# Performance work log

Measured on AMD Instinct MI355X. Metric: run time of the kernel, lower is better.

Reference implementation:

```python
import jax, jax.numpy as jnp
import numpy as np

NEG_SLOPE = 0.2  # PyG GATConv default leaky_relu slope


def gat_conv(x, ei, W, a_src, a_dst, b, heads, ch):
    """One PyG-style GATConv (eval mode, add_self_loops already applied to ei)."""
    N = x.shape[0]
    h = (x @ W).reshape(N, heads, ch)                      # [N,H,C]
    src, dst = ei[0], ei[1]
    al_s = jnp.sum(h * a_src, axis=-1)                     # [N,H]
    al_d = jnp.sum(h * a_dst, axis=-1)                     # [N,H]
    e = jax.nn.leaky_relu(al_s[src] + al_d[dst], NEG_SLOPE)  # [E,H]
    m = jax.ops.segment_max(e, dst, num_segments=N)        # stable softmax over in-edges
    ex = jnp.exp(e - m[dst])
    den = jax.ops.segment_sum(ex, dst, num_segments=N)
    alpha = ex / den[dst]                                  # [E,H]
    msg = alpha[:, :, None] * h[src]                       # [E,H,C]
    out = jax.ops.segment_sum(msg, dst, num_segments=N)    # [N,H,C]
    return out.reshape(N, heads * ch) + b


def setup_inputs() -> dict:
    key = jax.random.key(0)
    ks = jax.random.split(key, 12)
    N, E, D_in, C, H, D_out = 10000, 320000, 256, 128, 4, 64
    HC = H * C

    def glorot(k, shape):
        fan = shape[0] + shape[-1]
        return jax.random.normal(k, shape, dtype=jnp.float32) * np.sqrt(2.0 / fan)

    x = jax.random.normal(ks[0], (N, D_in), dtype=jnp.float32)
    edge_index = jax.random.randint(ks[1], (2, E), 0, N, dtype=jnp.int64)
    return {
        "x": x,
        "edge_index": edge_index,
        "W1": glorot(ks[2], (D_in, HC)),
        "a_src1": glorot(ks[3], (H, C)),
        "a_dst1": glorot(ks[4], (H, C)),
        "b1": jnp.zeros((HC,), dtype=jnp.float32),
        "W2": glorot(ks[5], (HC, HC)),
        "a_src2": glorot(ks[6], (H, C)),
        "a_dst2": glorot(ks[7], (H, C)),
        "b2": jnp.zeros((HC,), dtype=jnp.float32),
        "W3": glorot(ks[8], (HC, D_out)),
        "a_src3": glorot(ks[9], (1, D_out)),
        "a_dst3": glorot(ks[10], (1, D_out)),
        "b3": jnp.zeros((D_out,), dtype=jnp.float32),
    }


def reference(x, edge_index, W1, a_src1, a_dst1, b1, W2, a_src2, a_dst2, b2,
              W3, a_src3, a_dst3, b3):
    N = x.shape[0]
    loops = jnp.arange(N, dtype=edge_index.dtype)
    ei = jnp.concatenate([edge_index, jnp.stack([loops, loops])], axis=1)
    H, C = a_src1.shape
    h = jax.nn.elu(gat_conv(x, ei, W1, a_src1, a_dst1, b1, H, C))
    h = jax.nn.elu(gat_conv(h, ei, W2, a_src2, a_dst2, b2, H, C))
    out = gat_conv(h, ei, W3, a_src3, a_dst3, b3, 1, a_src3.shape[1])
    return out
```

## Files before the change

### kernel.cpp

```cpp
#include <hip/hip_runtime.h>
#include <hip/hip_fp16.h>

typedef _Float16 f16x8 __attribute__((ext_vector_type(8)));
typedef float f32x4 __attribute__((ext_vector_type(4)));

__device__ __forceinline__ unsigned short f2h_bits(float f) {
    __half h = __float2half(f);
    return *reinterpret_cast<unsigned short*>(&h);
}
__device__ __forceinline__ float h2f_bits(unsigned short u) {
    __half h = *reinterpret_cast<__half*>(&u);
    return __half2float(h);
}

__device__ __forceinline__ void fma_mix_lo(float& acc, float a, unsigned hw) {
    asm("v_fma_mix_f32 %0, %1, %2, %0 op_sel_hi:[0,1,0]"
        : "+v"(acc) : "v"(a), "v"(hw));
}
__device__ __forceinline__ void fma_mix_hi(float& acc, float a, unsigned hw) {
    asm("v_fma_mix_f32 %0, %1, %2, %0 op_sel:[0,1,0] op_sel_hi:[0,1,0]"
        : "+v"(acc) : "v"(a), "v"(hw));
}

__device__ __forceinline__ void gload_lds16(const void* g, void* l) {
    __builtin_amdgcn_global_load_lds(
        (const __attribute__((address_space(1))) unsigned int*)g,
        (__attribute__((address_space(3))) unsigned int*)l, 16, 0, 0);
}

__global__ void k_prep(const float* __restrict__ W1, unsigned short* __restrict__ W1T,
                       const float* __restrict__ W2, unsigned short* __restrict__ W2T,
                       const float* __restrict__ W3, unsigned short* __restrict__ W3T,
                       const float* __restrict__ x, unsigned short* __restrict__ xb,
                       int* __restrict__ csr, int Mcap,
                       const int* __restrict__ ei, int E, int* __restrict__ deg,
                       int DIN, int HC, int DOUT, int N)
{
    int i = blockIdx.x * blockDim.x + threadIdx.x;
    int n1 = DIN * HC;
    int n2 = n1 + HC * HC;
    int n3 = n2 + HC * DOUT;
    int n4 = n3 + N * DIN;
    int n5 = n4 + Mcap;
    int n6 = n5 + E;
    if (i < n1) {
        int k = i / HC, n = i - k * HC;
        W1T[n * DIN + k] = f2h_bits(W1[i]);
    } else if (i < n2) {
        int j = i - n1;
        int k = j / HC, n = j - k * HC;
        W2T[n * HC + k] = f2h_bits(W2[j]);
    } else if (i < n3) {
        int j = i - n2;
        int k = j / DOUT, n = j - k * DOUT;
        W3T[n * HC + k] = f2h_bits(W3[j]);
    } else if (i < n4) {
        int j = i - n3;
        xb[j] = f2h_bits(x[j]);
    } else if (i < n5) {
        csr[i - n4] = -1;
    } else if (i < n6) {
        atomicAdd(&deg[ei[E + (i - n5)]], 1);
    }
}

__global__ void k_scan(const int* __restrict__ deg, int* __restrict__ off,
                       int* __restrict__ cur, int N) {
    __shared__ int sums[1024];
    int t = threadIdx.x;
    int chunk = (N + 1023) >> 10;
    int lo = t * chunk;
    int hi = lo + chunk; if (hi > N) hi = N;
    if (lo > N) lo = N;
    int s = 0;
    for (int i = lo; i < hi; ++i) s += (deg[i] + 4) & ~3;
    sums[t] = s;
    __syncthreads();
    for (int dd = 1; dd < 1024; dd <<= 1) {
        int v = (t >= dd) ? sums[t - dd] : 0;
        __syncthreads();
        sums[t] += v;
        __syncthreads();
    }
    int run = sums[t] - s;
    for (int i = lo; i < hi; ++i) { off[i] = run; cur[i] = run; run += (deg[i] + 4) & ~3; }
    if (t == 1023) off[N] = run;
}
__global__ void k_fill(const int* __restrict__ ei, int E, int N,
                       int* cur, int* __restrict__ csr) {
    int i = blockIdx.x * blockDim.x + threadIdx.x;
    if (i < E) {
        int s = ei[i], d = ei[E + i];
        int pos = atomicAdd(&cur[d], 1);
        csr[pos] = s;
    } else if (i < E + N) {
        int nn = i - E;
        int pos = atomicAdd(&cur[nn], 1);
        csr[pos] = nn;
    }
}

template <bool OUTH, bool DOAL>
__global__ __launch_bounds__(256) void k_gemm(
    const unsigned short* __restrict__ A, const unsigned short* __restrict__ BT,
    void* __restrict__ D, int M, int K, int Nc, int tiles_n,
    const float* __restrict__ asrc, const float* __restrict__ adst,
    float* __restrict__ als, float* __restrict__ ald)
{
    int wid = blockIdx.x * (blockDim.x >> 6) + (threadIdx.x >> 6);
    int tiles_m = (M + 63) >> 6;
    if (wid >= tiles_m * tiles_n) return;
    int lane = threadIdx.x & 63;
    int tm = wid / tiles_n, tn = wid - tm * tiles_n;
    int m0 = tm << 6, n0 = tn << 6;
    int r = lane & 15, q = lane >> 4;

    const unsigned short* Arow[4];
    const unsigned short* Brow[4];
#pragma unroll
    for (int i = 0; i < 4; ++i) {
        int row = m0 + 16 * i + r; row = row < M ? row : M - 1;
        Arow[i] = A + (size_t)row * K + q * 8;
        Brow[i] = BT + (size_t)(n0 + 16 * i + r) * K + q * 8;
    }

    f32x4 acc[4][4] = {};
    f16x8 a[4], b[4], a2[4], b2[4];
#pragma unroll
    for (int i = 0; i < 4; ++i) {
        a[i] = *(const f16x8*)(Arow[i]);
        b[i] = *(const f16x8*)(Brow[i]);
    }
    for (int k0 = 0; k0 < K; k0 += 32) {
        int kn = k0 + 32;
        if (kn < K) {
#pragma unroll
            for (int i = 0; i < 4; ++i) {
                a2[i] = *(const f16x8*)(Arow[i] + kn);
                b2[i] = *(const f16x8*)(Brow[i] + kn);
            }
        }
#pragma unroll
        for (int i = 0; i < 4; ++i)
#pragma unroll
            for (int j = 0; j < 4; ++j)
                acc[i][j] = __builtin_amdgcn_mfma_f32_16x16x32_f16(a[i], b[j], acc[i][j], 0, 0, 0);
        if (kn < K) {
#pragma unroll
            for (int i = 0; i < 4; ++i) { a[i] = a2[i]; b[i] = b2[i]; }
        }
    }
#pragma unroll
    for (int i = 0; i < 4; ++i) {
        int rowb = m0 + 16 * i + q * 4;
#pragma unroll
        for (int rr = 0; rr < 4; ++rr) {
            int row = rowb + rr;
            if (row < M) {
#pragma unroll
                for (int j = 0; j < 4; ++j) {
                    int col = n0 + 16 * j + r;
                    if (OUTH)
                        ((unsigned short*)D)[(size_t)row * Nc + col] = f2h_bits(acc[i][j][rr]);
                    else
                        ((float*)D)[(size_t)row * Nc + col] = acc[i][j][rr];
                }
            }
        }
    }
    if (DOAL) {
        float asl[4], adl[4];
#pragma unroll
        for (int j = 0; j < 4; ++j) { asl[j] = asrc[16 * j + r]; adl[j] = adst[16 * j + r]; }
#pragma unroll
        for (int i = 0; i < 4; ++i) {
#pragma unroll
            for (int rr = 0; rr < 4; ++rr) {
                float s = 0.f, d = 0.f;
#pragma unroll
                for (int j = 0; j < 4; ++j) {
                    s += acc[i][j][rr] * asl[j];
                    d += acc[i][j][rr] * adl[j];
                }
#pragma unroll
                for (int dd = 1; dd < 16; dd <<= 1) {
                    s += __shfl_xor(s, dd);
                    d += __shfl_xor(d, dd);
                }
                int row = m0 + 16 * i + q * 4 + rr;
                if (r == 0 && row < M) { als[row] = s; ald[row] = d; }
            }
        }
    }
}

__global__ __launch_bounds__(256) void k_gemm_lds(
    const unsigned short* __restrict__ A, const unsigned short* __restrict__ BT,
    unsigned short* __restrict__ D, int M, int K, int Nc, int tiles_n)
{
    __shared__ unsigned short As[128 * 32];
    __shared__ unsigned short Bs[64 * 32];
    int tm = blockIdx.x / tiles_n, tn = blockIdx.x - tm * tiles_n;
    int m0 = tm << 7, n0 = tn << 6;
    int tid = threadIdx.x;
    int w = tid >> 6, lane = tid & 63;
    int wr = w >> 1, wc = w & 1;
    int r = lane & 15, q = lane >> 4;

    int lrow = lane >> 2;
    int lch = (lane & 3) * 8;
    int ga0 = m0 + w * 16 + lrow;       if (ga0 >= M) ga0 = M - 1;
    int ga1 = m0 + (w + 4) * 16 + lrow; if (ga1 >= M) ga1 = M - 1;
    const unsigned short* pa0 = A + (size_t)ga0 * K + lch;
    const unsigned short* pa1 = A + (size_t)ga1 * K + lch;
    const unsigned short* pb  = BT + (size_t)(n0 + w * 16 + lrow) * K + lch;
    unsigned short* lA0 = As + w * 512;
    unsigned short* lA1 = As + (w + 4) * 512;
    unsigned short* lB  = Bs + w * 512;

    const unsigned short* arp = As + (wr * 64 + r) * 32 + q * 8;
    const unsigned short* brp = Bs + (wc * 32 + r) * 32 + q * 8;

    f32x4 acc[4][2] = {};
    for (int k0 = 0; k0 < K; k0 += 32) {
        gload_lds16(pa0 + k0, lA0);
        gload_lds16(pa1 + k0, lA1);
        gload_lds16(pb + k0, lB);
        __syncthreads();
        f16x8 a[4], b[2];
#pragma unroll
        for (int i = 0; i < 4; ++i) a[i] = *(const f16x8*)(arp + i * 16 * 32);
#pragma unroll
        for (int j = 0; j < 2; ++j) b[j] = *(const f16x8*)(brp + j * 16 * 32);
#pragma unroll
        for (int i = 0; i < 4; ++i)
#pragma unroll
            for (int j = 0; j < 2; ++j)
                acc[i][j] = __builtin_amdgcn_mfma_f32_16x16x32_f16(a[i], b[j], acc[i][j], 0, 0, 0);
        __syncthreads();
    }
#pragma unroll
    for (int i = 0; i < 4; ++i) {
        int rowb = m0 + wr * 64 + 16 * i + q * 4;
#pragma unroll
        for (int rr = 0; rr < 4; ++rr) {
            int row = rowb + rr;
            if (row < M) {
#pragma unroll
                for (int j = 0; j < 2; ++j) {
                    int col = n0 + wc * 32 + 16 * j + r;
                    D[(size_t)row * Nc + col] = f2h_bits(acc[i][j][rr]);
                }
            }
        }
    }
}

template <int HCt, int Ht>
__global__ __launch_bounds__(256) void k_al(
    const unsigned short* __restrict__ h, const float* __restrict__ asrc,
    const float* __restrict__ adst,
    float* __restrict__ als, float* __restrict__ ald, int N)
{
    int wid = blockIdx.x * (blockDim.x >> 6) + (threadIdx.x >> 6);
    if (wid >= N) return;
    int lane = threadIdx.x & 63;
    const int CH = HCt / 64;
    const int Gs = 64 / Ht;
    float s = 0.f, d = 0.f;
    if constexpr (CH == 8) {
        const uint4* hr = (const uint4*)(h + (size_t)wid * HCt) + lane;
        uint4 hv = *hr;
        unsigned wds[4] = {hv.x, hv.y, hv.z, hv.w};
        const f32x4* as4 = (const f32x4*)(asrc + lane * 8);
        const f32x4* ad4 = (const f32x4*)(adst + lane * 8);
        f32x4 av0 = as4[0], av1 = as4[1], dv0 = ad4[0], dv1 = ad4[1];
#pragma unroll
        for (int wv = 0; wv < 4; ++wv) {
            float a0 = (wv < 2) ? av0[2 * wv] : av1[2 * (wv - 2)];
            float a1 = (wv < 2) ? av0[2 * wv + 1] : av1[2 * (wv - 2) + 1];
            float d0 = (wv < 2) ? dv0[2 * wv] : dv1[2 * (wv - 2)];
            float d1 = (wv < 2) ? dv0[2 * wv + 1] : dv1[2 * (wv - 2) + 1];
            fma_mix_lo(s, a0, wds[wv]); fma_mix_hi(s, a1, wds[wv]);
            fma_mix_lo(d, d0, wds[wv]); fma_mix_hi(d, d1, wds[wv]);
        }
    } else {
        float hv = h2f_bits(h[(size_t)wid * HCt + lane]);
        s = hv * asrc[lane];
        d = hv * adst[lane];
    }
#pragma unroll
    for (int dd = 1; dd < Gs; dd <<= 1) {
        s += __shfl_xor(s, dd);
        d += __shfl_xor(d, dd);
    }
    if ((lane & (Gs - 1)) == 0) {
        int hh = lane / Gs;
        als[wid * Ht + hh] = s;
        ald[wid * Ht + hh] = d;
    }
}

template <bool DOELU>
__global__ __launch_bounds__(256) void k_aggr4d(
    const unsigned short* __restrict__ h, const float* __restrict__ als,
    const float* __restrict__ ald,
    const int* __restrict__ off, const int* __restrict__ csr,
    const float* __restrict__ bias,
    unsigned short* __restrict__ outp, int N)
{
    __shared__ float alpS[4][4][64];
    int wid = threadIdx.x >> 6;
    int n = blockIdx.x * 4 + wid;
    if (n >= N) return;
    int lane = threadIdx.x & 63;
    int g4 = lane >> 4;

    int off0 = off[n], off1 = off[n + 1];
    int degp = off1 - off0;
    const int4* csr4 = (const int4*)(csr + off0);
    f32x4 ald4 = *(const f32x4*)(ald + (size_t)n * 4);

    float acc[8] = {};
    float den = 0.f;
    const char* hB = (const char*)h;
    const unsigned offp = (unsigned)(lane * 16);

    for (int base = 0; base < degp; base += 64) {
        f32x4 av = {0.f, 0.f, 0.f, 0.f};
        int e = base + lane;
        if (e < degp) {
            int s = csr[off0 + e];
            if (s >= 0) {
                f32x4 a4 = *(const f32x4*)(als + (size_t)(unsigned)s * 4);
#pragma unroll
                for (int hh = 0; hh < 4; ++hh) {
                    float l = a4[hh] + ald4[hh];
                    l = l > 0.f ? l : 0.2f * l;
                    av[hh] = __expf(l);
                }
            }
        }
#pragma unroll
        for (int hh = 0; hh < 4; ++hh) alpS[wid][hh][lane] = av[hh];

        int qn = (degp - base) >> 2; if (qn > 16) qn = 16;
        int qb = base >> 2;
        for (int qq = 0; qq < qn; ++qq) {
            int4 cs = csr4[qb + qq];
            f32x4 af = *(const f32x4*)&alpS[wid][g4][qq * 4];
            int c0 = cs.x < 0 ? 0 : cs.x;
            int c1 = cs.y < 0 ? 0 : cs.y;
            int c2 = cs.z < 0 ? 0 : cs.z;
            int c3 = cs.w < 0 ? 0 : cs.w;
            uint4 h0 = *(const uint4*)(hB + (size_t)((((unsigned)c0) << 10) + offp));
            uint4 h1 = *(const uint4*)(hB + (size_t)((((unsigned)c1) << 10) + offp));
            uint4 h2 = *(const uint4*)(hB + (size_t)((((unsigned)c2) << 10) + offp));
            uint4 h3 = *(const uint4*)(hB + (size_t)((((unsigned)c3) << 10) + offp));
            den += (af[0] + af[1]) + (af[2] + af[3]);
            unsigned w0[4] = {h0.x, h0.y, h0.z, h0.w};
            unsigned w1[4] = {h1.x, h1.y, h1.z, h1.w};
            unsigned w2[4] = {h2.x, h2.y, h2.z, h2.w};
            unsigned w3[4] = {h3.x, h3.y, h3.z, h3.w};
#pragma unroll
            for (int wv = 0; wv < 4; ++wv) {
                fma_mix_lo(acc[2 * wv],     af[0], w0[wv]);
                fma_mix_hi(acc[2 * wv + 1], af[0], w0[wv]);
            }
#pragma unroll
            for (int wv = 0; wv < 4; ++wv) {
                fma_mix_lo(acc[2 * wv],     af[1], w1[wv]);
                fma_mix_hi(acc[2 * wv + 1], af[1], w1[wv]);
            }
#pragma unroll
            for (int wv = 0; wv < 4; ++wv) {
                fma_mix_lo(acc[2 * wv],     af[2], w2[wv]);
                fma_mix_hi(acc[2 * wv + 1], af[2], w2[wv]);
            }
#pragma unroll
            for (int wv = 0; wv < 4; ++wv) {
                fma_mix_lo(acc[2 * wv],     af[3], w3[wv]);
                fma_mix_hi(acc[2 * wv + 1], af[3], w3[wv]);
            }
        }
    }

    float inv = 1.f / den;
    int cb = lane * 8;
    const f32x4* b4 = (const f32x4*)(bias + cb);
    f32x4 bv0 = b4[0], bv1 = b4[1];
    unsigned ww[4];
#pragma unroll
    for (int wv = 0; wv < 4; ++wv) {
        float v0 = acc[2 * wv] * inv + (wv < 2 ? bv0[2 * wv] : bv1[2 * (wv - 2)]);
        float v1 = acc[2 * wv + 1] * inv + (wv < 2 ? bv0[2 * wv + 1] : bv1[2 * (wv - 2) + 1]);
        if (DOELU) {
            v0 = v0 > 0.f ? v0 : expm1f(v0);
            v1 = v1 > 0.f ? v1 : expm1f(v1);
        }
        ww[wv] = (unsigned)f2h_bits(v0) | ((unsigned)f2h_bits(v1) << 16);
    }
    uint4 o; o.x = ww[0]; o.y = ww[1]; o.z = ww[2]; o.w = ww[3];
    *((uint4*)(outp + (size_t)n * 512 + cb)) = o;
}

__global__ __launch_bounds__(256) void k_aggr1b(
    const unsigned short* __restrict__ h, const float* __restrict__ als,
    const float* __restrict__ aldv, const int* __restrict__ off,
    const int* __restrict__ csr, const float* __restrict__ bias,
    float* __restrict__ outp, int N)
{
    int n = blockIdx.x * (blockDim.x >> 6) + (threadIdx.x >> 6);
    if (n >= N) return;
    int lane = threadIdx.x & 63;
    int g = lane >> 4;
    int p = lane & 15;
    int q0 = (off[n] >> 2) + g, q1 = off[n + 1] >> 2;
    float aldh = aldv[n];

    float acc[4] = {};
    float den = 0.f;
    const char* hB = (const char*)h;
    const unsigned offp = (unsigned)(p * 8);
    const int4* csr4 = (const int4*)csr;

    auto aof = [&](int ss) -> float {
        int sc = ss < 0 ? 0 : ss;
        float l = als[sc] + aldh;
        l = l > 0.f ? l : 0.2f * l;
        float e = __expf(l);
        return ss < 0 ? 0.f : e;
    };
    auto fmaq = [&](float a, const uint2& hq) {
        den += a;
        fma_mix_lo(acc[0], a, hq.x);
        fma_mix_hi(acc[1], a, hq.x);
        fma_mix_lo(acc[2], a, hq.y);
        fma_mix_hi(acc[3], a, hq.y);
    };

    for (int q = q0; q < q1; q += 4) {
        int4 cs = csr4[q];
        float a0 = aof(cs.x), a1 = aof(cs.y), a2 = aof(cs.z), a3 = aof(cs.w);
        uint2 h0 = *(const uint2*)(hB + (size_t)((((unsigned)(cs.x < 0 ? 0 : cs.x)) << 7) + offp));
        uint2 h1 = *(const uint2*)(hB + (size_t)((((unsigned)(cs.y < 0 ? 0 : cs.y)) << 7) + offp));
        uint2 h2 = *(const uint2*)(hB + (size_t)((((unsigned)(cs.z < 0 ? 0 : cs.z)) << 7) + offp));
        uint2 h3 = *(const uint2*)(hB + (size_t)((((unsigned)(cs.w < 0 ? 0 : cs.w)) << 7) + offp));
        fmaq(a0, h0);
        fmaq(a1, h1);
        fmaq(a2, h2);
        fmaq(a3, h3);
    }

    den += __shfl_xor(den, 16);
    den += __shfl_xor(den, 32);
#pragma unroll
    for (int j = 0; j < 4; ++j) {
        acc[j] += __shfl_xor(acc[j], 16);
        acc[j] += __shfl_xor(acc[j], 32);
    }
    if (g == 0) {
        float inv = 1.f / den;
        f32x4 o;
#pragma unroll
        for (int j = 0; j < 4; ++j)
            o[j] = acc[j] * inv + bias[p * 4 + j];
        *((f32x4*)(outp + (size_t)n * 64 + p * 4)) = o;
    }
}

extern "C" void kernel_launch(void* const* d_in, const int* in_sizes, int n_in,
                              void* d_out, int out_size, void* d_ws, size_t ws_size,
                              hipStream_t stream)
{
    const float* x   = (const float*)d_in[0];
    const int*   ei  = (const int*)d_in[1];
    const float* W1  = (const float*)d_in[2];
    const float* as1 = (const float*)d_in[3];
    const float* ad1 = (const float*)d_in[4];
    const float* b1  = (const float*)d_in[5];
    const float* W2  = (const float*)d_in[6];
    const float* as2 = (const float*)d_in[7];
    const float* ad2 = (const float*)d_in[8];
    const float* b2  = (const float*)d_in[9];
    const float* W3  = (const float*)d_in[10];
    const float* as3 = (const float*)d_in[11];
    const float* ad3 = (const float*)d_in[12];
    const float* b3  = (const float*)d_in[13];

    const int DIN = 256, HC = 512, DOUT = 64;
    int N = in_sizes[0] / DIN;
    int E = in_sizes[1] / 2;
    int Mcap = E + 4 * N;

    char* w = (char*)d_ws;
    auto alloc = [&](size_t bytes) -> char* {
        char* p = w;
        w += (bytes + 255) & ~(size_t)255;
        return p;
    };
    int* deg    = (int*)alloc((size_t)N * 4);
    int* cur    = (int*)alloc((size_t)N * 4);
    int* off    = (int*)alloc((size_t)(N + 1) * 4);
    int* csr    = (int*)alloc((size_t)Mcap * 4);
    unsigned short* W1T = (unsigned short*)alloc((size_t)HC * DIN * 2);
    unsigned short* W2T = (unsigned short*)alloc((size_t)HC * HC * 2);
    unsigned short* W3T = (unsigned short*)alloc((size_t)DOUT * HC * 2);
    unsigned short* xb  = (unsigned short*)alloc((size_t)N * DIN * 2);
    unsigned short* act = (unsigned short*)alloc((size_t)N * HC * 2);
    unsigned short* hb  = (unsigned short*)alloc((size_t)N * HC * 2);
    unsigned short* hb3 = (unsigned short*)alloc((size_t)N * DOUT * 2);
    float* als   = (float*)alloc((size_t)N * 4 * 4);
    float* ald   = (float*)alloc((size_t)N * 4 * 4);

    hipMemsetAsync(deg, 0, (size_t)N * 4, stream);
    int prep_total = DIN * HC + HC * HC + HC * DOUT + N * DIN + Mcap + E;
    k_prep<<<(prep_total + 255) / 256, 256, 0, stream>>>(
        W1, W1T, W2, W2T, W3, W3T, x, xb, csr, Mcap, ei, E, deg, DIN, HC, DOUT, N);
    k_scan<<<1, 1024, 0, stream>>>(deg, off, cur, N);
    k_fill<<<(E + N + 255) / 256, 256, 0, stream>>>(ei, E, N, cur, csr);

    int tiles_m = (N + 63) / 64;
    auto gemm_blocks = [&](int tn) { return (tiles_m * tn + 3) / 4; };
    int tm128 = (N + 127) / 128;
    int nwave_blocks = (N + 3) / 4;
    int nodeBlocks = (N + 3) / 4;

    k_gemm_lds<<<tm128 * (HC / 64), 256, 0, stream>>>(xb, W1T, hb, N, DIN, HC, HC / 64);
    k_al<512, 4><<<nwave_blocks, 256, 0, stream>>>(hb, as1, ad1, als, ald, N);
    k_aggr4d<true><<<nodeBlocks, 256, 0, stream>>>(hb, als, ald, off, csr, b1, act, N);

    k_gemm_lds<<<tm128 * (HC / 64), 256, 0, stream>>>(act, W2T, hb, N, HC, HC, HC / 64);
    k_al<512, 4><<<nwave_blocks, 256, 0, stream>>>(hb, as2, ad2, als, ald, N);
    k_aggr4d<true><<<nodeBlocks, 256, 0, stream>>>(hb, als, ald, off, csr, b2, act, N);

    k_gemm<true, true><<<gemm_blocks(1), 256, 0, stream>>>(
        act, W3T, hb3, N, HC, DOUT, 1, as3, ad3, als, ald);
    k_aggr1b<<<nwave_blocks, 256, 0, stream>>>(hb3, als, ald, off, csr, b3, (float*)d_out, N);
}
```

Before: 283.9 us.

## Split 4-head aggregation across blocks per head, lane groups over edges

The aggregation kernel for the two 4-head layers is restructured so that each block handles one head. Each wave's four 16-lane groups stride over edge quads in parallel, and partial sums are combined with cross-group shuffles. This gives 4x more blocks and more independent gathers in flight per wave, aiming to hide gather latency. In exchange the CSR indices and softmax logits are re-read once per head, and the final reduction adds shuffles.

```diff
diff --git a/kernel.cpp b/kernel.cpp
--- a/kernel.cpp
+++ b/kernel.cpp
@@ -302,53 +302,51 @@
 }
 
 template <bool DOELU>
-__global__ __launch_bounds__(256) void k_aggr4d(
+__global__ __launch_bounds__(256) void k_aggr4e(
     const unsigned short* __restrict__ h, const float* __restrict__ als,
     const float* __restrict__ ald,
     const int* __restrict__ off, const int* __restrict__ csr,
     const float* __restrict__ bias,
-    unsigned short* __restrict__ outp, int N)
-{
-    __shared__ float alpS[4][4][64];
+    unsigned short* __restrict__ outp, int N, int nodeBlocks)
+{
+    __shared__ float alpS[4][64];
+    int head = blockIdx.x / nodeBlocks;
+    int nb = blockIdx.x - head * nodeBlocks;
     int wid = threadIdx.x >> 6;
-    int n = blockIdx.x * 4 + wid;
+    int n = nb * 4 + wid;
     if (n >= N) return;
     int lane = threadIdx.x & 63;
-    int g4 = lane >> 4;
-
-    int off0 = off[n], off1 = off[n + 1];
-    int degp = off1 - off0;
+    int g = lane >> 4;
+    int p = lane & 15;
+
+    int off0 = off[n];
+    int degp = off[n + 1] - off0;
+    float aldh = ald[n * 4 + head];
+    const char* hB = (const char*)h;
+    const unsigned offp = (unsigned)(head * 256 + p * 16);
     const int4* csr4 = (const int4*)(csr + off0);
-    f32x4 ald4 = *(const f32x4*)(ald + (size_t)n * 4);
 
     float acc[8] = {};
     float den = 0.f;
-    const char* hB = (const char*)h;
-    const unsigned offp = (unsigned)(lane * 16);
 
     for (int base = 0; base < degp; base += 64) {
-        f32x4 av = {0.f, 0.f, 0.f, 0.f};
+        float av = 0.f;
         int e = base + lane;
         if (e < degp) {
             int s = csr[off0 + e];
             if (s >= 0) {
-                f32x4 a4 = *(const f32x4*)(als + (size_t)(unsigned)s * 4);
-#pragma unroll
-                for (int hh = 0; hh < 4; ++hh) {
-                    float l = a4[hh] + ald4[hh];
-                    l = l > 0.f ? l : 0.2f * l;
-                    av[hh] = __expf(l);
-                }
-            }
-        }
-#pragma unroll
-        for (int hh = 0; hh < 4; ++hh) alpS[wid][hh][lane] = av[hh];
+                float l = als[(size_t)(unsigned)s * 4 + head] + aldh;
+                l = l > 0.f ? l : 0.2f * l;
+                av = __expf(l);
+            }
+        }
+        alpS[wid][lane] = av;
 
         int qn = (degp - base) >> 2; if (qn > 16) qn = 16;
         int qb = base >> 2;
-        for (int qq = 0; qq < qn; ++qq) {
+        for (int qq = g; qq < qn; qq += 4) {
             int4 cs = csr4[qb + qq];
-            f32x4 af = *(const f32x4*)&alpS[wid][g4][qq * 4];
+            f32x4 af = *(const f32x4*)&alpS[wid][qq * 4];
             int c0 = cs.x < 0 ? 0 : cs.x;
             int c1 = cs.y < 0 ? 0 : cs.y;
             int c2 = cs.z < 0 ? 0 : cs.z;
@@ -385,23 +383,31 @@
         }
     }
 
-    float inv = 1.f / den;
-    int cb = lane * 8;
-    const f32x4* b4 = (const f32x4*)(bias + cb);
-    f32x4 bv0 = b4[0], bv1 = b4[1];
-    unsigned ww[4];
-#pragma unroll
-    for (int wv = 0; wv < 4; ++wv) {
-        float v0 = acc[2 * wv] * inv + (wv < 2 ? bv0[2 * wv] : bv1[2 * (wv - 2)]);
-        float v1 = acc[2 * wv + 1] * inv + (wv < 2 ? bv0[2 * wv + 1] : bv1[2 * (wv - 2) + 1]);
-        if (DOELU) {
-            v0 = v0 > 0.f ? v0 : expm1f(v0);
-            v1 = v1 > 0.f ? v1 : expm1f(v1);
-        }
-        ww[wv] = (unsigned)f2h_bits(v0) | ((unsigned)f2h_bits(v1) << 16);
-    }
-    uint4 o; o.x = ww[0]; o.y = ww[1]; o.z = ww[2]; o.w = ww[3];
-    *((uint4*)(outp + (size_t)n * 512 + cb)) = o;
+    den += __shfl_xor(den, 16);
+    den += __shfl_xor(den, 32);
+#pragma unroll
+    for (int j = 0; j < 8; ++j) {
+        acc[j] += __shfl_xor(acc[j], 16);
+        acc[j] += __shfl_xor(acc[j], 32);
+    }
+
+    if (g == 0) {
+        float inv = 1.f / den;
+        int cb = head * 128 + p * 8;
+        unsigned ww[4];
+#pragma unroll
+        for (int wv = 0; wv < 4; ++wv) {
+            float v0 = acc[2 * wv] * inv + bias[cb + 2 * wv];
+            float v1 = acc[2 * wv + 1] * inv + bias[cb + 2 * wv + 1];
+            if (DOELU) {
+                v0 = v0 > 0.f ? v0 : expm1f(v0);
+                v1 = v1 > 0.f ? v1 : expm1f(v1);
+            }
+            ww[wv] = (unsigned)f2h_bits(v0) | ((unsigned)f2h_bits(v1) << 16);
+        }
+        uint4 o; o.x = ww[0]; o.y = ww[1]; o.z = ww[2]; o.w = ww[3];
+        *((uint4*)(outp + (size_t)n * 512 + cb)) = o;
+    }
 }
 
 __global__ __launch_bounds__(256) void k_aggr1b(
@@ -528,11 +534,11 @@
 
     k_gemm_lds<<<tm128 * (HC / 64), 256, 0, stream>>>(xb, W1T, hb, N, DIN, HC, HC / 64);
     k_al<512, 4><<<nwave_blocks, 256, 0, stream>>>(hb, as1, ad1, als, ald, N);
-    k_aggr4d<true><<<nodeBlocks, 256, 0, stream>>>(hb, als, ald, off, csr, b1, act, N);
+    k_aggr4e<true><<<4 * nodeBlocks, 256, 0, stream>>>(hb, als, ald, off, csr, b1, act, N, nodeBlocks);
 
     k_gemm_lds<<<tm128 * (HC / 64), 256, 0, stream>>>(act, W2T, hb, N, HC, HC, HC / 64);
     k_al<512, 4><<<nwave_blocks, 256, 0, stream>>>(hb, as2, ad2, als, ald, N);
-    k_aggr4d<true><<<nodeBlocks, 256, 0, stream>>>(hb, als, ald, off, csr, b2, act, N);
+    k_aggr4e<true><<<4 * nodeBlocks, 256, 0, stream>>>(hb, als, ald, off, csr, b2, act, N, nodeBlocks);
 
     k_gemm<true, true><<<gemm_blocks(1), 256, 0, stream>>>(
         act, W3T, hb3, N, HC, DOUT, 1, as3, ad3, als, ald);
```

Measured after the change: 283.4 us. Within noise of the previous version (-0.2%).
